# Optimization experiments

Measured on AMD Instinct MI355X. Metric: run time of the kernel, lower is better.

## Reference

```python
import jax, jax.numpy as jnp
import numpy as np

WT, WH, WW = 2, 8, 8
N_WIN = WT * WH * WW  # 128 tokens per window
DIM, HEADS = 192, 6
HEAD_DIM = DIM // HEADS
SCALE = HEAD_DIM ** -0.5


def _relative_position_index():
    ct, ch, cw = np.arange(WT), np.arange(WH), np.arange(WW)
    coords = np.stack(np.meshgrid(ct, ch, cw, indexing='ij'))  # (3,WT,WH,WW)
    cf = coords.reshape(3, -1)
    rel = cf[:, :, None] - cf[:, None, :]  # (3,N,N)
    rel = rel.transpose(1, 2, 0).copy()
    rel[:, :, 0] += WT - 1
    rel[:, :, 1] += WH - 1
    rel[:, :, 2] += WW - 1
    rel[:, :, 0] *= (2 * WH - 1) * (2 * WW - 1)
    rel[:, :, 1] *= 2 * WW - 1
    return rel.sum(-1)  # (N,N) int

_REL_IDX = jnp.asarray(_relative_position_index())


def _layernorm(x, g, b, eps=1e-5):
    mu = x.mean(-1, keepdims=True)
    var = ((x - mu) ** 2).mean(-1, keepdims=True)
    return (x - mu) * jax.lax.rsqrt(var + eps) * g + b


def setup_inputs() -> dict:
    key = jax.random.key(0)
    ks = jax.random.split(key, 16)
    B, T, H, W, C = 2, 8, 128, 128, DIM
    hid = 4 * C
    n_bias = (2 * WT - 1) * (2 * WH - 1) * (2 * WW - 1)
    s = lambda fan: 1.0 / np.sqrt(fan)
    return {
        'x': jax.random.normal(ks[0], (B, T, H, W, C), jnp.float32),
        'norm1_g': jnp.ones((C,), jnp.float32),
        'norm1_b': jnp.zeros((C,), jnp.float32),
        'qkv_w': jax.random.normal(ks[1], (3 * C, C), jnp.float32) * s(C),
        'qkv_b': jnp.zeros((3 * C,), jnp.float32),
        'bias_table': jax.random.normal(ks[2], (n_bias, HEADS), jnp.float32) * 0.02,
        'proj_w': jax.random.normal(ks[3], (C, C), jnp.float32) * s(C),
        'proj_b': jnp.zeros((C,), jnp.float32),
        'norm2_g': jnp.ones((C,), jnp.float32),
        'norm2_b': jnp.zeros((C,), jnp.float32),
        'fc1_w': jax.random.normal(ks[4], (hid, C), jnp.float32) * s(C),
        'fc1_b': jnp.zeros((hid,), jnp.float32),
        'fc2_w': jax.random.normal(ks[5], (C, hid), jnp.float32) * s(hid),
        'fc2_b': jnp.zeros((C,), jnp.float32),
    }


def reference(x, norm1_g, norm1_b, qkv_w, qkv_b, bias_table, proj_w, proj_b,
              norm2_g, norm2_b, fc1_w, fc1_b, fc2_w, fc2_b):
    B, T, H, W, C = x.shape
    shortcut = x
    xn = _layernorm(x, norm1_g, norm1_b)

    # window partition: (B,T,H,W,C) -> (B_, N, C)
    xw = xn.reshape(B, T // WT, WT, H // WH, WH, W // WW, WW, C)
    xw = xw.transpose(0, 1, 3, 5, 2, 4, 6, 7).reshape(-1, N_WIN, C)

    # qkv projection (torch Linear: y = x @ W.T + b)
    qkv = xw @ qkv_w.T + qkv_b  # (B_, N, 3C)
    B_ = qkv.shape[0]
    qkv = qkv.reshape(B_, N_WIN, 3, HEADS, HEAD_DIM)
    q, k, v = qkv[:, :, 0], qkv[:, :, 1], qkv[:, :, 2]  # (B_, N, h, d)

    attn = jnp.einsum('bnhd,bmhd->bhnm', q * SCALE, k)
    bias = bias_table[_REL_IDX.reshape(-1)].reshape(N_WIN, N_WIN, HEADS)
    attn = attn + bias.transpose(2, 0, 1)[None]  # (B_, h, N, N)
    attn = jax.nn.softmax(attn, axis=-1)

    out = jnp.einsum('bhnm,bmhd->bnhd', attn, v).reshape(B_, N_WIN, C)
    out = out @ proj_w.T + proj_b

    # window reverse
    out = out.reshape(B, T // WT, H // WH, W // WW, WT, WH, WW, C)
    out = out.transpose(0, 1, 4, 2, 5, 3, 6, 7).reshape(B, T, H, W, C)

    x = shortcut + out
    # MLP with residual (GELU exact, matching nn.GELU default)
    h1 = _layernorm(x, norm2_g, norm2_b) @ fc1_w.T + fc1_b
    h1 = jax.nn.gelu(h1, approximate=False)
    x = x + (h1 @ fc2_w.T + fc2_b)
    return x
```

## Files before the change

kernel.cpp:

```cpp
#include <hip/hip_runtime.h>
#include <hip/hip_bf16.h>
#include <math.h>

typedef __hip_bfloat16 bf16;
typedef __attribute__((ext_vector_type(8))) __bf16 bf16x8;
typedef __attribute__((ext_vector_type(4))) float floatx4;

#define CDIM 192
#define N_WINDOWS 2048
#define ATT_SCALE 0.17677669529663687f

__device__ inline float toF(float v) { return v; }
__device__ inline float toF(bf16 v) { return __bfloat162float(v); }

__device__ inline long nat_index(int wi, int n, int col) {
    int wb = wi & 15, hb = (wi >> 4) & 15, tb = (wi >> 8) & 3, bb = wi >> 10;
    int t  = tb * 2 + (n >> 6);
    int hh = hb * 8 + ((n >> 3) & 7);
    int w  = wb * 8 + (n & 7);
    return ((((long)(bb * 8 + t)) * 128 + hh) * 128 + w) * CDIM + col;
}

__launch_bounds__(256)
__global__ void cvt_w_kernel(const float* __restrict__ src, bf16* __restrict__ dst, int n) {
    int i = (blockIdx.x * 256 + threadIdx.x) * 8;
    if (i < n) {
        float4 a = *(const float4*)(src + i);
        float4 b = *(const float4*)(src + i + 4);
        bf16x8 o;
        o[0] = (__bf16)a.x; o[1] = (__bf16)a.y; o[2] = (__bf16)a.z; o[3] = (__bf16)a.w;
        o[4] = (__bf16)b.x; o[5] = (__bf16)b.y; o[6] = (__bf16)b.z; o[7] = (__bf16)b.w;
        *(bf16x8*)(dst + i) = o;
    }
}

template<bool WINDOWED, typename T>
__launch_bounds__(256)
__global__ void ln_kernel(const T* __restrict__ x, const float* __restrict__ g,
                          const float* __restrict__ bta, bf16* __restrict__ out,
                          int wi_base) {
    int row = blockIdx.x * 4 + (threadIdx.x >> 6);
    int lane = threadIdx.x & 63;
    long src;
    if (WINDOWED) {
        src = nat_index(wi_base + (row >> 7), row & 127, 0);
    } else {
        src = (long)row * CDIM;
    }
    float v0 = toF(x[src + lane]);
    float v1 = toF(x[src + lane + 64]);
    float v2 = toF(x[src + lane + 128]);
    float s = v0 + v1 + v2;
    float sq = v0 * v0 + v1 * v1 + v2 * v2;
    #pragma unroll
    for (int o = 32; o > 0; o >>= 1) { s += __shfl_xor(s, o); sq += __shfl_xor(sq, o); }
    float mean = s * (1.0f / 192.0f);
    float var  = sq * (1.0f / 192.0f) - mean * mean;
    float rstd = rsqrtf(fmaxf(var, 0.0f) + 1e-5f);
    long dst = (long)row * CDIM;
    out[dst + lane]       = __float2bfloat16((v0 - mean) * rstd * g[lane]       + bta[lane]);
    out[dst + lane + 64]  = __float2bfloat16((v1 - mean) * rstd * g[lane + 64]  + bta[lane + 64]);
    out[dst + lane + 128] = __float2bfloat16((v2 - mean) * rstd * g[lane + 128] + bta[lane + 128]);
}

template<typename Epi>
__launch_bounds__(256)
__global__ void gemm_bt(const bf16* __restrict__ A, const bf16* __restrict__ Wt,
                        int K, Epi epi) {
    __shared__ __align__(16) bf16 sA[128 * 32];
    __shared__ __align__(16) bf16 sW[64 * 32];
    const int tid = threadIdx.x;
    const int lane = tid & 63;
    const int wv = tid >> 6;
    const int m0 = blockIdx.x * 128;
    const int n0 = blockIdx.y * 64;

    floatx4 acc[2][4] = {};

    for (int k0 = 0; k0 < K; k0 += 32) {
        #pragma unroll
        for (int i = 0; i < 2; ++i) {
            int idx = tid + i * 256;
            int row = idx >> 2, kc = (idx & 3) << 3;
            *(uint4*)(&sA[row * 32 + kc]) =
                *(const uint4*)(A + (long)(m0 + row) * K + k0 + kc);
        }
        {
            int row = tid >> 2, kc = (tid & 3) << 3;
            *(uint4*)(&sW[row * 32 + kc]) =
                *(const uint4*)(Wt + (long)(n0 + row) * K + k0 + kc);
        }
        __syncthreads();
        bf16x8 aF[2], bF[4];
        #pragma unroll
        for (int rt = 0; rt < 2; ++rt)
            aF[rt] = *(const bf16x8*)(&sA[(wv * 32 + rt * 16 + (lane & 15)) * 32 + (lane >> 4) * 8]);
        #pragma unroll
        for (int ct = 0; ct < 4; ++ct)
            bF[ct] = *(const bf16x8*)(&sW[(ct * 16 + (lane & 15)) * 32 + (lane >> 4) * 8]);
        #pragma unroll
        for (int rt = 0; rt < 2; ++rt)
            #pragma unroll
            for (int ct = 0; ct < 4; ++ct)
                acc[rt][ct] = __builtin_amdgcn_mfma_f32_16x16x32_bf16(aF[rt], bF[ct], acc[rt][ct], 0, 0, 0);
        __syncthreads();
    }
    #pragma unroll
    for (int rt = 0; rt < 2; ++rt)
        #pragma unroll
        for (int ct = 0; ct < 4; ++ct)
            #pragma unroll
            for (int r = 0; r < 4; ++r) {
                int row = m0 + wv * 32 + rt * 16 + (lane >> 4) * 4 + r;
                int col = n0 + ct * 16 + (lane & 15);
                epi(row, col, acc[rt][ct][r]);
            }
}

struct EpiQKV {
    const float* bias; bf16 *q, *k, *v;
    __device__ void operator()(int row, int col, float val) const {
        val += bias[col];
        int wi = row >> 7, n = row & 127;
        int part = col / 192, rem = col - part * 192;
        int h = rem >> 5, d = rem & 31;
        long base = (long)(wi * 6 + h);
        if (part == 0)      q[(base * 128 + n) * 32 + d] = __float2bfloat16(val);
        else if (part == 1) k[(base * 128 + n) * 32 + d] = __float2bfloat16(val);
        else                v[(base * 32 + d) * 128 + n] = __float2bfloat16(val);
    }
};

struct EpiProj {
    const float* bias; const float* x; bf16* x2; int wi_base;
    __device__ void operator()(int row, int col, float val) const {
        val += bias[col];
        long nat = nat_index(wi_base + (row >> 7), row & 127, col);
        x2[(long)row * CDIM + col] = __float2bfloat16(val + x[nat]);
    }
};

struct EpiGelu {
    const float* bias; bf16* h1;
    __device__ void operator()(int row, int col, float val) const {
        val += bias[col];
        float g = 0.5f * val * (1.0f + erff(val * 0.70710678118654752f));
        h1[(long)row * 768 + col] = __float2bfloat16(g);
    }
};

struct EpiOut {
    const float* bias; const bf16* x2; float* out; int wi_base;
    __device__ void operator()(int row, int col, float val) const {
        val += bias[col];
        long nat = nat_index(wi_base + (row >> 7), row & 127, col);
        out[nat] = val + __bfloat162float(x2[(long)row * CDIM + col]);
    }
};

__device__ inline float rel_bias(const float* bt, int h, int n, int m) {
    int tn = n >> 6, hn = (n >> 3) & 7, wn = n & 7;
    int tm = m >> 6, hm = (m >> 3) & 7, wm = m & 7;
    int idx = (tn - tm + 1) * 225 + (hn - hm + 7) * 15 + (wn - wm + 7);
    return bt[idx * 6 + h];
}

__launch_bounds__(256)
__global__ void attn_kernel(const bf16* __restrict__ q, const bf16* __restrict__ k,
                            const bf16* __restrict__ vT, const float* __restrict__ bt,
                            bf16* __restrict__ out) {
    __shared__ __align__(16) bf16 sQ[128 * 32];
    __shared__ __align__(16) bf16 sK[128 * 32];
    __shared__ __align__(16) bf16 sVT[32 * 128];
    __shared__ __align__(16) bf16 sP[128 * 128];
    const int blk = blockIdx.x;
    const int h = blk % 6;
    const int wi = blk / 6;
    const int tid = threadIdx.x, lane = tid & 63, wv = tid >> 6;
    const bf16* qg = q + (long)blk * 4096;
    const bf16* kg = k + (long)blk * 4096;
    const bf16* vg = vT + (long)blk * 4096;
    #pragma unroll
    for (int i = 0; i < 2; ++i) {
        int idx = (tid + i * 256) * 8;
        *(uint4*)(&sQ[idx])  = *(const uint4*)(qg + idx);
        *(uint4*)(&sK[idx])  = *(const uint4*)(kg + idx);
        *(uint4*)(&sVT[idx]) = *(const uint4*)(vg + idx);
    }
    __syncthreads();

    const int mrow = wv * 32;
    const int colb = lane & 15, quad = lane >> 4;
    floatx4 zero = {0.f, 0.f, 0.f, 0.f};
    floatx4 s[2][8];
    bf16x8 aF[2];
    #pragma unroll
    for (int rt = 0; rt < 2; ++rt)
        aF[rt] = *(const bf16x8*)(&sQ[(mrow + rt * 16 + colb) * 32 + quad * 8]);
    #pragma unroll
    for (int ct = 0; ct < 8; ++ct) {
        bf16x8 bF = *(const bf16x8*)(&sK[(ct * 16 + colb) * 32 + quad * 8]);
        #pragma unroll
        for (int rt = 0; rt < 2; ++rt)
            s[rt][ct] = __builtin_amdgcn_mfma_f32_16x16x32_bf16(aF[rt], bF, zero, 0, 0, 0);
    }
    #pragma unroll
    for (int rt = 0; rt < 2; ++rt) {
        #pragma unroll
        for (int r = 0; r < 4; ++r) {
            int n = mrow + rt * 16 + quad * 4 + r;
            float vals[8];
            float mx = -1e30f;
            #pragma unroll
            for (int ct = 0; ct < 8; ++ct) {
                float v = s[rt][ct][r] * ATT_SCALE + rel_bias(bt, h, n, ct * 16 + colb);
                vals[ct] = v; mx = fmaxf(mx, v);
            }
            #pragma unroll
            for (int o = 1; o < 16; o <<= 1) mx = fmaxf(mx, __shfl_xor(mx, o));
            float sum = 0.f;
            #pragma unroll
            for (int ct = 0; ct < 8; ++ct) { vals[ct] = __expf(vals[ct] - mx); sum += vals[ct]; }
            #pragma unroll
            for (int o = 1; o < 16; o <<= 1) sum += __shfl_xor(sum, o);
            float inv = 1.0f / sum;
            #pragma unroll
            for (int ct = 0; ct < 8; ++ct)
                sP[n * 128 + ct * 16 + colb] = __float2bfloat16(vals[ct] * inv);
        }
    }
    __syncthreads();
    floatx4 o[2][2] = {};
    #pragma unroll
    for (int kk = 0; kk < 4; ++kk) {
        bf16x8 aP[2];
        #pragma unroll
        for (int rt = 0; rt < 2; ++rt)
            aP[rt] = *(const bf16x8*)(&sP[(mrow + rt * 16 + colb) * 128 + kk * 32 + quad * 8]);
        #pragma unroll
        for (int ct = 0; ct < 2; ++ct) {
            bf16x8 bV = *(const bf16x8*)(&sVT[(ct * 16 + colb) * 128 + kk * 32 + quad * 8]);
            #pragma unroll
            for (int rt = 0; rt < 2; ++rt)
                o[rt][ct] = __builtin_amdgcn_mfma_f32_16x16x32_bf16(aP[rt], bV, o[rt][ct], 0, 0, 0);
        }
    }
    #pragma unroll
    for (int rt = 0; rt < 2; ++rt)
        #pragma unroll
        for (int ct = 0; ct < 2; ++ct)
            #pragma unroll
            for (int r = 0; r < 4; ++r) {
                int n = mrow + rt * 16 + quad * 4 + r;
                out[((long)(wi * 128 + n)) * CDIM + h * 32 + ct * 16 + colb] =
                    __float2bfloat16(o[rt][ct][r]);
            }
}

extern "C" void kernel_launch(void* const* d_in, const int* in_sizes, int n_in,
                              void* d_out, int out_size, void* d_ws, size_t ws_size,
                              hipStream_t stream) {
    const float* x      = (const float*)d_in[0];
    const float* n1g    = (const float*)d_in[1];
    const float* n1b    = (const float*)d_in[2];
    const float* qkv_w  = (const float*)d_in[3];
    const float* qkv_b  = (const float*)d_in[4];
    const float* btab   = (const float*)d_in[5];
    const float* proj_w = (const float*)d_in[6];
    const float* proj_b = (const float*)d_in[7];
    const float* n2g    = (const float*)d_in[8];
    const float* n2b    = (const float*)d_in[9];
    const float* fc1_w  = (const float*)d_in[10];
    const float* fc1_b  = (const float*)d_in[11];
    const float* fc2_w  = (const float*)d_in[12];
    const float* fc2_b  = (const float*)d_in[13];
    float* outp = (float*)d_out;

    char* ws = (char*)d_ws;

    const int NQKV = 576 * 192, NPROJ = 192 * 192, NFC1 = 768 * 192, NFC2 = 192 * 768;
    bf16* qkvW = (bf16*)ws;
    bf16* projW = qkvW + NQKV;
    bf16* fc1W = projW + NPROJ;
    bf16* fc2W = fc1W + NFC1;
    const size_t WBYTES = (size_t)(NQKV + NPROJ + NFC1 + NFC2) * 2;

    cvt_w_kernel<<<NQKV / 2048, 256, 0, stream>>>(qkv_w, qkvW, NQKV);
    cvt_w_kernel<<<NPROJ / 2048, 256, 0, stream>>>(proj_w, projW, NPROJ);
    cvt_w_kernel<<<NFC1 / 2048, 256, 0, stream>>>(fc1_w, fc1W, NFC1);
    cvt_w_kernel<<<NFC2 / 2048, 256, 0, stream>>>(fc2_w, fc2W, NFC2);

    const size_t per_win = 6UL * 128 * 192 * 2;
    size_t avail = ws_size > WBYTES ? ws_size - WBYTES : 0;
    int S = 512;
    while (S > 64 && (size_t)S * per_win > avail) S >>= 1;

    char* slots = ws + WBYTES;
    const size_t SLOT = (size_t)S * 128 * CDIM * 2;
    bf16* bufA = (bf16*)(slots);
    bf16* qb   = (bf16*)(slots + SLOT);
    bf16* kb   = (bf16*)(slots + 2 * SLOT);
    bf16* vb   = (bf16*)(slots + 3 * SLOT);
    bf16* x2   = qb;
    bf16* h1   = kb;

    for (int s0 = 0; s0 < N_WINDOWS; s0 += S) {
        ln_kernel<true, float><<<S * 32, 256, 0, stream>>>(x, n1g, n1b, bufA, s0);
        gemm_bt<EpiQKV><<<dim3(S, 9), 256, 0, stream>>>(bufA, qkvW, 192, EpiQKV{qkv_b, qb, kb, vb});
        attn_kernel<<<S * 6, 256, 0, stream>>>(qb, kb, vb, btab, bufA);
        gemm_bt<EpiProj><<<dim3(S, 3), 256, 0, stream>>>(bufA, projW, 192, EpiProj{proj_b, x, x2, s0});
        ln_kernel<false, bf16><<<S * 32, 256, 0, stream>>>(x2, n2g, n2b, bufA, 0);
        gemm_bt<EpiGelu><<<dim3(S, 12), 256, 0, stream>>>(bufA, fc1W, 192, EpiGelu{fc1_b, h1});
        gemm_bt<EpiOut><<<dim3(S, 3), 256, 0, stream>>>(h1, fc2W, 768, EpiOut{fc2_b, x2, outp, s0});
    }
}
```

Before: 1.675 ms.

## Load full-K GEMM tiles via direct-to-LDS, swizzle LDS, precompute attention bias

```diff
diff --git a/kernel.cpp b/kernel.cpp
--- a/kernel.cpp
+++ b/kernel.cpp
@@ -12,6 +12,12 @@
 
 __device__ inline float toF(float v) { return v; }
 __device__ inline float toF(bf16 v) { return __bfloat162float(v); }
+
+__device__ inline void gld16(const void* g, void* l) {
+    __builtin_amdgcn_global_load_lds((const __attribute__((address_space(1))) uint32_t*)g,
+                                     (__attribute__((address_space(3))) uint32_t*)l,
+                                     16, 0, 0);
+}
 
 __device__ inline long nat_index(int wi, int n, int col) {
     int wb = wi & 15, hb = (wi >> 4) & 15, tb = (wi >> 8) & 3, bb = wi >> 10;
@@ -32,6 +38,22 @@
         o[4] = (__bf16)b.x; o[5] = (__bf16)b.y; o[6] = (__bf16)b.z; o[7] = (__bf16)b.w;
         *(bf16x8*)(dst + i) = o;
     }
+}
+
+__device__ inline float rel_bias(const float* bt, int h, int n, int m) {
+    int tn = n >> 6, hn = (n >> 3) & 7, wn = n & 7;
+    int tm = m >> 6, hm = (m >> 3) & 7, wm = m & 7;
+    int idx = (tn - tm + 1) * 225 + (hn - hm + 7) * 15 + (wn - wm + 7);
+    return bt[idx * 6 + h];
+}
+
+__launch_bounds__(256)
+__global__ void bias_expand_kernel(const float* __restrict__ bt, float* __restrict__ bias6) {
+    int i = blockIdx.x * 256 + threadIdx.x;
+    int n = i >> 7, m = i & 127;
+    #pragma unroll
+    for (int h = 0; h < 6; ++h)
+        bias6[h * 16384 + i] = rel_bias(bt, h, n, m);
 }
 
 template<bool WINDOWED, typename T>
@@ -64,57 +86,71 @@
 }
 
 template<typename Epi>
-__launch_bounds__(256)
+__launch_bounds__(256, 2)
 __global__ void gemm_bt(const bf16* __restrict__ A, const bf16* __restrict__ Wt,
-                        int K, Epi epi) {
-    __shared__ __align__(16) bf16 sA[128 * 32];
-    __shared__ __align__(16) bf16 sW[64 * 32];
+                        int K, int nb, Epi epi) {
+    __shared__ __align__(16) bf16 sA[128 * 192];
+    __shared__ __align__(16) bf16 sW[64 * 192];
     const int tid = threadIdx.x;
     const int lane = tid & 63;
     const int wv = tid >> 6;
-    const int m0 = blockIdx.x * 128;
-    const int n0 = blockIdx.y * 64;
-
+    int gid = blockIdx.x;
+    int swz = (gid & 7) * (gridDim.x >> 3) + (gid >> 3);
+    const int m0 = (swz / nb) * 128;
+    const int n0 = (swz % nb) * 64;
+
+    const int colb = lane & 15, quad = lane >> 4;
     floatx4 acc[2][4] = {};
 
-    for (int k0 = 0; k0 < K; k0 += 32) {
-        #pragma unroll
-        for (int i = 0; i < 2; ++i) {
-            int idx = tid + i * 256;
-            int row = idx >> 2, kc = (idx & 3) << 3;
-            *(uint4*)(&sA[row * 32 + kc]) =
-                *(const uint4*)(A + (long)(m0 + row) * K + k0 + kc);
-        }
-        {
-            int row = tid >> 2, kc = (tid & 3) << 3;
-            *(uint4*)(&sW[row * 32 + kc]) =
-                *(const uint4*)(Wt + (long)(n0 + row) * K + k0 + kc);
+    for (int k0 = 0; k0 < K; k0 += 192) {
+        if (k0) __syncthreads();
+        #pragma unroll
+        for (int i = 0; i < 12; ++i) {
+            int t = i * 256 + tid;
+            int r = t / 24, cb = (t - r * 24) * 16;
+            int scb = cb ^ ((r & 7) << 4);
+            gld16((const char*)(A + (long)(m0 + r) * K + k0) + scb,
+                  (char*)sA + i * 4096 + wv * 1024);
+        }
+        #pragma unroll
+        for (int i = 0; i < 6; ++i) {
+            int t = i * 256 + tid;
+            int r = t / 24, cb = (t - r * 24) * 16;
+            int scb = cb ^ ((r & 7) << 4);
+            gld16((const char*)(Wt + (long)(n0 + r) * K + k0) + scb,
+                  (char*)sW + i * 4096 + wv * 1024);
         }
         __syncthreads();
-        bf16x8 aF[2], bF[4];
-        #pragma unroll
-        for (int rt = 0; rt < 2; ++rt)
-            aF[rt] = *(const bf16x8*)(&sA[(wv * 32 + rt * 16 + (lane & 15)) * 32 + (lane >> 4) * 8]);
-        #pragma unroll
-        for (int ct = 0; ct < 4; ++ct)
-            bF[ct] = *(const bf16x8*)(&sW[(ct * 16 + (lane & 15)) * 32 + (lane >> 4) * 8]);
-        #pragma unroll
-        for (int rt = 0; rt < 2; ++rt)
+        #pragma unroll
+        for (int kk = 0; kk < 6; ++kk) {
+            bf16x8 aF[2], bF[4];
+            int cb = kk * 64 + quad * 16;
+            #pragma unroll
+            for (int rt = 0; rt < 2; ++rt) {
+                int rr = wv * 32 + rt * 16 + colb;
+                aF[rt] = *(const bf16x8*)((char*)sA + rr * 384 + (cb ^ ((rr & 7) << 4)));
+            }
+            #pragma unroll
+            for (int ct = 0; ct < 4; ++ct) {
+                int rr = ct * 16 + colb;
+                bF[ct] = *(const bf16x8*)((char*)sW + rr * 384 + (cb ^ ((rr & 7) << 4)));
+            }
+            #pragma unroll
+            for (int rt = 0; rt < 2; ++rt)
+                #pragma unroll
+                for (int ct = 0; ct < 4; ++ct)
+                    acc[rt][ct] = __builtin_amdgcn_mfma_f32_16x16x32_bf16(aF[rt], bF[ct], acc[rt][ct], 0, 0, 0);
+        }
+    }
+    #pragma unroll
+    for (int rt = 0; rt < 2; ++rt)
+        #pragma unroll
+        for (int r = 0; r < 4; ++r) {
+            int row = m0 + wv * 32 + rt * 16 + quad * 4 + r;
             #pragma unroll
             for (int ct = 0; ct < 4; ++ct)
-                acc[rt][ct] = __builtin_amdgcn_mfma_f32_16x16x32_bf16(aF[rt], bF[ct], acc[rt][ct], 0, 0, 0);
-        __syncthreads();
-    }
-    #pragma unroll
-    for (int rt = 0; rt < 2; ++rt)
-        #pragma unroll
-        for (int ct = 0; ct < 4; ++ct)
-            #pragma unroll
-            for (int r = 0; r < 4; ++r) {
-                int row = m0 + wv * 32 + rt * 16 + (lane >> 4) * 4 + r;
-                int col = n0 + ct * 16 + (lane & 15);
-                epi(row, col, acc[rt][ct][r]);
-            }
+                epi(row, n0 + ct * 16 + colb, acc[rt][ct][r]);
+        }
 }
 
 struct EpiQKV {
@@ -125,7 +161,7 @@
         int part = col / 192, rem = col - part * 192;
         int h = rem >> 5, d = rem & 31;
         long base = (long)(wi * 6 + h);
-        if (part == 0)      q[(base * 128 + n) * 32 + d] = __float2bfloat16(val);
+        if (part == 0)      q[(base * 128 + n) * 32 + d] = __float2bfloat16(val * ATT_SCALE);
         else if (part == 1) k[(base * 128 + n) * 32 + d] = __float2bfloat16(val);
         else                v[(base * 32 + d) * 128 + n] = __float2bfloat16(val);
     }
@@ -158,16 +194,9 @@
     }
 };
 
-__device__ inline float rel_bias(const float* bt, int h, int n, int m) {
-    int tn = n >> 6, hn = (n >> 3) & 7, wn = n & 7;
-    int tm = m >> 6, hm = (m >> 3) & 7, wm = m & 7;
-    int idx = (tn - tm + 1) * 225 + (hn - hm + 7) * 15 + (wn - wm + 7);
-    return bt[idx * 6 + h];
-}
-
 __launch_bounds__(256)
 __global__ void attn_kernel(const bf16* __restrict__ q, const bf16* __restrict__ k,
-                            const bf16* __restrict__ vT, const float* __restrict__ bt,
+                            const bf16* __restrict__ vT, const float* __restrict__ bias6,
                             bf16* __restrict__ out) {
     __shared__ __align__(16) bf16 sQ[128 * 32];
     __shared__ __align__(16) bf16 sK[128 * 32];
@@ -182,10 +211,14 @@
     const bf16* vg = vT + (long)blk * 4096;
     #pragma unroll
     for (int i = 0; i < 2; ++i) {
-        int idx = (tid + i * 256) * 8;
-        *(uint4*)(&sQ[idx])  = *(const uint4*)(qg + idx);
-        *(uint4*)(&sK[idx])  = *(const uint4*)(kg + idx);
-        *(uint4*)(&sVT[idx]) = *(const uint4*)(vg + idx);
+        int t = tid + i * 256;
+        int r = t >> 2, cb = (t & 3) << 4;
+        int d = r * 64 + (cb ^ ((r & 6) << 3));
+        *(uint4*)((char*)sQ + d) = *(const uint4*)(qg + t * 8);
+        *(uint4*)((char*)sK + d) = *(const uint4*)(kg + t * 8);
+        int rv = t >> 4, cv = (t & 15) << 4;
+        int dv = rv * 256 + (cv ^ ((rv & 7) << 4));
+        *(uint4*)((char*)sVT + dv) = *(const uint4*)(vg + t * 8);
     }
     __syncthreads();
 
@@ -195,15 +228,19 @@
     floatx4 s[2][8];
     bf16x8 aF[2];
     #pragma unroll
-    for (int rt = 0; rt < 2; ++rt)
-        aF[rt] = *(const bf16x8*)(&sQ[(mrow + rt * 16 + colb) * 32 + quad * 8]);
+    for (int rt = 0; rt < 2; ++rt) {
+        int rr = mrow + rt * 16 + colb;
+        aF[rt] = *(const bf16x8*)((char*)sQ + rr * 64 + ((quad * 16) ^ ((rr & 6) << 3)));
+    }
     #pragma unroll
     for (int ct = 0; ct < 8; ++ct) {
-        bf16x8 bF = *(const bf16x8*)(&sK[(ct * 16 + colb) * 32 + quad * 8]);
+        int rr = ct * 16 + colb;
+        bf16x8 bF = *(const bf16x8*)((char*)sK + rr * 64 + ((quad * 16) ^ ((rr & 6) << 3)));
         #pragma unroll
         for (int rt = 0; rt < 2; ++rt)
             s[rt][ct] = __builtin_amdgcn_mfma_f32_16x16x32_bf16(aF[rt], bF, zero, 0, 0, 0);
     }
+    const float* bh = bias6 + h * 16384;
     #pragma unroll
     for (int rt = 0; rt < 2; ++rt) {
         #pragma unroll
@@ -213,7 +250,7 @@
             float mx = -1e30f;
             #pragma unroll
             for (int ct = 0; ct < 8; ++ct) {
-                float v = s[rt][ct][r] * ATT_SCALE + rel_bias(bt, h, n, ct * 16 + colb);
+                float v = s[rt][ct][r] + bh[n * 128 + ct * 16 + colb];
                 vals[ct] = v; mx = fmaxf(mx, v);
             }
             #pragma unroll
@@ -225,21 +262,28 @@
             for (int o = 1; o < 16; o <<= 1) sum += __shfl_xor(sum, o);
             float inv = 1.0f / sum;
             #pragma unroll
-            for (int ct = 0; ct < 8; ++ct)
-                sP[n * 128 + ct * 16 + colb] = __float2bfloat16(vals[ct] * inv);
+            for (int ct = 0; ct < 8; ++ct) {
+                int cwb = (ct * 16 + colb) * 2;
+                *(bf16*)((char*)sP + n * 256 + (cwb ^ ((n & 7) << 4))) =
+                    __float2bfloat16(vals[ct] * inv);
+            }
         }
     }
     __syncthreads();
     floatx4 o[2][2] = {};
     #pragma unroll
     for (int kk = 0; kk < 4; ++kk) {
+        int cbb = kk * 64 + quad * 16;
         bf16x8 aP[2];
         #pragma unroll
-        for (int rt = 0; rt < 2; ++rt)
-            aP[rt] = *(const bf16x8*)(&sP[(mrow + rt * 16 + colb) * 128 + kk * 32 + quad * 8]);
+        for (int rt = 0; rt < 2; ++rt) {
+            int rr = mrow + rt * 16 + colb;
+            aP[rt] = *(const bf16x8*)((char*)sP + rr * 256 + (cbb ^ ((rr & 7) << 4)));
+        }
         #pragma unroll
         for (int ct = 0; ct < 2; ++ct) {
-            bf16x8 bV = *(const bf16x8*)(&sVT[(ct * 16 + colb) * 128 + kk * 32 + quad * 8]);
+            int rr = ct * 16 + colb;
+            bf16x8 bV = *(const bf16x8*)((char*)sVT + rr * 256 + (cbb ^ ((rr & 7) << 4)));
             #pragma unroll
             for (int rt = 0; rt < 2; ++rt)
                 o[rt][ct] = __builtin_amdgcn_mfma_f32_16x16x32_bf16(aP[rt], bV, o[rt][ct], 0, 0, 0);
@@ -284,18 +328,21 @@
     bf16* fc1W = projW + NPROJ;
     bf16* fc2W = fc1W + NFC1;
     const size_t WBYTES = (size_t)(NQKV + NPROJ + NFC1 + NFC2) * 2;
+    float* bias6 = (float*)(ws + WBYTES);
+    const size_t BBYTES = 6UL * 128 * 128 * 4;
 
     cvt_w_kernel<<<NQKV / 2048, 256, 0, stream>>>(qkv_w, qkvW, NQKV);
     cvt_w_kernel<<<NPROJ / 2048, 256, 0, stream>>>(proj_w, projW, NPROJ);
     cvt_w_kernel<<<NFC1 / 2048, 256, 0, stream>>>(fc1_w, fc1W, NFC1);
     cvt_w_kernel<<<NFC2 / 2048, 256, 0, stream>>>(fc2_w, fc2W, NFC2);
+    bias_expand_kernel<<<64, 256, 0, stream>>>(btab, bias6);
 
     const size_t per_win = 6UL * 128 * 192 * 2;
-    size_t avail = ws_size > WBYTES ? ws_size - WBYTES : 0;
+    size_t avail = ws_size > WBYTES + BBYTES ? ws_size - WBYTES - BBYTES : 0;
     int S = 512;
     while (S > 64 && (size_t)S * per_win > avail) S >>= 1;
 
-    char* slots = ws + WBYTES;
+    char* slots = ws + WBYTES + BBYTES;
     const size_t SLOT = (size_t)S * 128 * CDIM * 2;
     bf16* bufA = (bf16*)(slots);
     bf16* qb   = (bf16*)(slots + SLOT);
@@ -306,11 +353,11 @@
 
     for (int s0 = 0; s0 < N_WINDOWS; s0 += S) {
         ln_kernel<true, float><<<S * 32, 256, 0, stream>>>(x, n1g, n1b, bufA, s0);
-        gemm_bt<EpiQKV><<<dim3(S, 9), 256, 0, stream>>>(bufA, qkvW, 192, EpiQKV{qkv_b, qb, kb, vb});
-        attn_kernel<<<S * 6, 256, 0, stream>>>(qb, kb, vb, btab, bufA);
-        gemm_bt<EpiProj><<<dim3(S, 3), 256, 0, stream>>>(bufA, projW, 192, EpiProj{proj_b, x, x2, s0});
+        gemm_bt<EpiQKV><<<S * 9, 256, 0, stream>>>(bufA, qkvW, 192, 9, EpiQKV{qkv_b, qb, kb, vb});
+        attn_kernel<<<S * 6, 256, 0, stream>>>(qb, kb, vb, bias6, bufA);
+        gemm_bt<EpiProj><<<S * 3, 256, 0, stream>>>(bufA, projW, 192, 3, EpiProj{proj_b, x, x2, s0});
         ln_kernel<false, bf16><<<S * 32, 256, 0, stream>>>(x2, n2g, n2b, bufA, 0);
-        gemm_bt<EpiGelu><<<dim3(S, 12), 256, 0, stream>>>(bufA, fc1W, 192, EpiGelu{fc1_b, h1});
-        gemm_bt<EpiOut><<<dim3(S, 3), 256, 0, stream>>>(h1, fc2W, 768, EpiOut{fc2_b, x2, outp, s0});
-    }
-}
+        gemm_bt<EpiGelu><<<S * 12, 256, 0, stream>>>(bufA, fc1W, 192, 12, EpiGelu{fc1_b, h1});
+        gemm_bt<EpiOut><<<S * 3, 256, 0, stream>>>(h1, fc2W, 768, 3, EpiOut{fc2_b, x2, outp, s0});
+    }
+}
```

After: 1.755 ms. 1.05x slower.
